# Performance work log

Hardware: AMD Instinct MI355X
Metric: run time of the kernel (lower is better)

## Reference

```python
import jax, jax.numpy as jnp
import numpy as np

N, M, D, G = 8192, 8192, 512, 10

def _embed_distance_matrix(dist):
    # classical MDS embedding: ||e_i - e_j||^2 == dist[i,j]**2
    g = dist.shape[0]
    d2 = dist ** 2
    J = np.eye(g) - np.ones((g, g)) / g
    B = -0.5 * J @ d2 @ J
    w, v = np.linalg.eigh(B)
    w = np.clip(w, 0.0, None)
    return (v * np.sqrt(w)).astype(np.float32)  # [g, g]

def setup_inputs() -> dict:
    key = jax.random.key(0)
    k1, k2, k3, k4 = jax.random.split(key, 4)
    X = jax.random.normal(k1, (N, D), dtype=jnp.float32)
    Z = jax.random.normal(k2, (M, D), dtype=jnp.float32)
    groupsX = jax.random.randint(k3, (N,), 0, G)
    groupsZ = jax.random.randint(k4, (M,), 0, G)
    group_distances = np.ones((G, G)) - np.eye(G)
    embedding = jnp.asarray(_embed_distance_matrix(group_distances))
    return {
        "X": X, "Z": Z,
        "groupsX": groupsX, "groupsZ": groupsZ,
        "embedding": embedding,
        "sigma": jnp.float32(1.0),
        "lengthscale": jnp.float32(1.0),
        "group_diff_param": jnp.float32(1.0),
    }

def _pairwise_sqdist(a, b):
    # ||a_i - b_j||^2 via GEMM; avoids the O(N*M*d) diff tensor
    aa = jnp.sum(a * a, axis=-1)  # [N]
    bb = jnp.sum(b * b, axis=-1)  # [M]
    return aa[:, None] + bb[None, :] - 2.0 * (a @ b.T)  # [N, M]

def reference(X, Z, groupsX, groupsZ, embedding, sigma, lengthscale, group_diff_param):
    p = X.shape[-1]
    ex = embedding[groupsX]  # [N, g]
    ez = embedding[groupsZ]  # [M, g]
    dist = _pairwise_sqdist(X, Z)           # [N, M]
    gdist = _pairwise_sqdist(ex, ez)        # [N, M]
    val = 1.0 / (jnp.abs(group_diff_param) * gdist + 1.0)
    dist_scaled = dist / lengthscale ** 2
    K = sigma ** 2 * jnp.exp(-0.5 * dist_scaled * val) * val ** (0.5 * p)
    return K  # [N, M], matches torch result.transpose(-1, 0)
```

## Files before the change

kernel.cpp:

```cpp
#include <hip/hip_runtime.h>
#include <hip/hip_bf16.h>
#include <cstdint>
#include <cstddef>

#define NROWS 8192
#define MCOLS 8192
#define DDIM  512
#define GRP   10

using bf16x8 = __attribute__((ext_vector_type(8))) short;
using f32x4  = __attribute__((ext_vector_type(4))) float;

typedef const __attribute__((address_space(1))) void* gas_ptr;
typedef __attribute__((address_space(3))) void* las_ptr;

__global__ void prep_tables(const float* __restrict__ emb,
                            const float* __restrict__ sigma_p,
                            const float* __restrict__ ls_p,
                            const float* __restrict__ gdp_p,
                            float* __restrict__ t_tab,
                            float* __restrict__ c2_tab) {
    int t = threadIdx.x;
    if (t >= GRP * GRP) return;
    int a = t / GRP, b = t % GRP;
    float gd = 0.0f;
    for (int g = 0; g < GRP; ++g) {
        float d = emb[a * GRP + g] - emb[b * GRP + g];
        gd += d * d;
    }
    float val = 1.0f / (fabsf(*gdp_p) * gd + 1.0f);
    float ls = *ls_p;
    float sg = *sigma_p;
    t_tab[t]  = -0.5f * val / (ls * ls);
    c2_tab[t] = sg * sg * powf(val, 0.5f * (float)DDIM);
}

__global__ __launch_bounds__(256) void prep_rows(const float* __restrict__ X,
                                                 const float* __restrict__ Z,
                                                 __hip_bfloat16* __restrict__ Xb,
                                                 __hip_bfloat16* __restrict__ Zb,
                                                 float* __restrict__ xx,
                                                 float* __restrict__ zz) {
    int row = blockIdx.x;
    const float* src;
    __hip_bfloat16* dst;
    float* sums;
    int r;
    if (row < NROWS) {
        r = row; src = X + (size_t)r * DDIM; dst = Xb + (size_t)r * DDIM; sums = xx;
    } else {
        r = row - NROWS; src = Z + (size_t)r * DDIM; dst = Zb + (size_t)r * DDIM; sums = zz;
    }
    int t = threadIdx.x;
    float a = src[t];
    float b = src[t + 256];
    dst[t]       = __float2bfloat16(a);
    dst[t + 256] = __float2bfloat16(b);
    float s = a * a + b * b;
    #pragma unroll
    for (int off = 32; off > 0; off >>= 1) s += __shfl_down(s, off, 64);
    __shared__ float ws[4];
    if ((t & 63) == 0) ws[t >> 6] = s;
    __syncthreads();
    if (t == 0) sums[r] = ws[0] + ws[1] + ws[2] + ws[3];
}

__global__ __launch_bounds__(256) void mggp_gemm(
    const __hip_bfloat16* __restrict__ Xb, const __hip_bfloat16* __restrict__ Zb,
    const float* __restrict__ xx, const float* __restrict__ zz,
    const int* __restrict__ gX, const int* __restrict__ gZ,
    const float* __restrict__ t_tab, const float* __restrict__ c2_tab,
    float* __restrict__ out) {

    __shared__ __align__(16) short Al[1024 * 8];
    __shared__ __align__(16) short Bl[1024 * 8];

    const int tid  = threadIdx.x;
    const int lane = tid & 63;
    const int w    = tid >> 6;
    const int wr   = w >> 1;
    const int wc   = w & 1;
    const int m    = lane & 15;
    const int q    = lane >> 4;

    const int brow = blockIdx.y * 128;
    const int bcol = blockIdx.x * 128;

    f32x4 acc[4][4];
    #pragma unroll
    for (int ti = 0; ti < 4; ++ti)
        #pragma unroll
        for (int tj = 0; tj < 4; ++tj)
            #pragma unroll
            for (int e = 0; e < 4; ++e) acc[ti][tj][e] = 0.0f;

    for (int kt = 0; kt < DDIM / 64; ++kt) {
        __syncthreads();
        #pragma unroll
        for (int p = 0; p < 4; ++p) {
            int sbase = (w * 4 + p) * 64;
            int s = sbase + lane;
            int r = s >> 3;
            int o = (s & 7) ^ (r & 7);
            const __hip_bfloat16* ga = Xb + (size_t)(brow + r) * DDIM + kt * 64 + o * 8;
            __builtin_amdgcn_global_load_lds((gas_ptr)ga, (las_ptr)&Al[sbase * 8], 16, 0, 0);
            const __hip_bfloat16* gb = Zb + (size_t)(bcol + r) * DDIM + kt * 64 + o * 8;
            __builtin_amdgcn_global_load_lds((gas_ptr)gb, (las_ptr)&Bl[sbase * 8], 16, 0, 0);
        }
        __syncthreads();

        #pragma unroll
        for (int kk = 0; kk < 2; ++kk) {
            bf16x8 aF[4], bF[4];
            #pragma unroll
            for (int ti = 0; ti < 4; ++ti) {
                int r = wr * 64 + ti * 16 + m;
                int o = kk * 4 + q;
                aF[ti] = *(const bf16x8*)&Al[(r * 8 + (o ^ (r & 7))) * 8];
            }
            #pragma unroll
            for (int tj = 0; tj < 4; ++tj) {
                int r = wc * 64 + tj * 16 + m;
                int o = kk * 4 + q;
                bF[tj] = *(const bf16x8*)&Bl[(r * 8 + (o ^ (r & 7))) * 8];
            }
            #pragma unroll
            for (int ti = 0; ti < 4; ++ti)
                #pragma unroll
                for (int tj = 0; tj < 4; ++tj)
                    acc[ti][tj] = __builtin_amdgcn_mfma_f32_16x16x32_bf16(
                        aF[ti], bF[tj], acc[ti][tj], 0, 0, 0);
        }
    }

    float zzv[4];
    int   gbv[4];
    #pragma unroll
    for (int tj = 0; tj < 4; ++tj) {
        int j = bcol + wc * 64 + tj * 16 + m;
        zzv[tj] = zz[j];
        gbv[tj] = gZ[j];
    }
    #pragma unroll
    for (int ti = 0; ti < 4; ++ti) {
        #pragma unroll
        for (int rg = 0; rg < 4; ++rg) {
            int i = brow + wr * 64 + ti * 16 + q * 4 + rg;
            float xxi = xx[i];
            int   ga  = gX[i] * GRP;
            float* orow = out + (size_t)i * MCOLS + bcol + wc * 64 + m;
            #pragma unroll
            for (int tj = 0; tj < 4; ++tj) {
                float dot  = acc[ti][tj][rg];
                float dist = xxi + zzv[tj] - 2.0f * dot;
                int   idx  = ga + gbv[tj];
                orow[tj * 16] = c2_tab[idx] * expf(dist * t_tab[idx]);
            }
        }
    }
}

extern "C" void kernel_launch(void* const* d_in, const int* in_sizes, int n_in,
                              void* d_out, int out_size, void* d_ws, size_t ws_size,
                              hipStream_t stream) {
    const float* X     = (const float*)d_in[0];
    const float* Z     = (const float*)d_in[1];
    const int*   gX    = (const int*)d_in[2];
    const int*   gZ    = (const int*)d_in[3];
    const float* emb   = (const float*)d_in[4];
    const float* sigma = (const float*)d_in[5];
    const float* ls    = (const float*)d_in[6];
    const float* gdp   = (const float*)d_in[7];

    char* ws = (char*)d_ws;
    const size_t XB_OFF  = 0;
    const size_t ZB_OFF  = XB_OFF + (size_t)NROWS * DDIM * 2;
    const size_t XX_OFF  = ZB_OFF + (size_t)MCOLS * DDIM * 2;
    const size_t ZZ_OFF  = XX_OFF + (size_t)NROWS * 4;
    const size_t TT_OFF  = ZZ_OFF + (size_t)MCOLS * 4;
    const size_t C2_OFF  = TT_OFF + 512;

    __hip_bfloat16* Xb = (__hip_bfloat16*)(ws + XB_OFF);
    __hip_bfloat16* Zb = (__hip_bfloat16*)(ws + ZB_OFF);
    float* xx    = (float*)(ws + XX_OFF);
    float* zz    = (float*)(ws + ZZ_OFF);
    float* t_tab = (float*)(ws + TT_OFF);
    float* c2tab = (float*)(ws + C2_OFF);

    prep_tables<<<1, 128, 0, stream>>>(emb, sigma, ls, gdp, t_tab, c2tab);
    prep_rows<<<2 * NROWS, 256, 0, stream>>>(X, Z, Xb, Zb, xx, zz);
    dim3 grid(MCOLS / 128, NROWS / 128);
    mggp_gemm<<<grid, 256, 0, stream>>>(Xb, Zb, xx, zz, gX, gZ, t_tab, c2tab,
                                        (float*)d_out);
}
```

Measured before the change: 405.0 us.

## Fuse prep kernels, vectorize row prep, swizzle GEMM tiles, use fast exp

```diff
diff --git a/kernel.cpp b/kernel.cpp
--- a/kernel.cpp
+++ b/kernel.cpp
@@ -14,34 +14,36 @@
 typedef const __attribute__((address_space(1))) void* gas_ptr;
 typedef __attribute__((address_space(3))) void* las_ptr;
 
-__global__ void prep_tables(const float* __restrict__ emb,
-                            const float* __restrict__ sigma_p,
-                            const float* __restrict__ ls_p,
-                            const float* __restrict__ gdp_p,
-                            float* __restrict__ t_tab,
-                            float* __restrict__ c2_tab) {
+__global__ __launch_bounds__(256) void prep_all(const float* __restrict__ X,
+                                                const float* __restrict__ Z,
+                                                __hip_bfloat16* __restrict__ Xb,
+                                                __hip_bfloat16* __restrict__ Zb,
+                                                float* __restrict__ xx,
+                                                float* __restrict__ zz,
+                                                const float* __restrict__ emb,
+                                                const float* __restrict__ sigma_p,
+                                                const float* __restrict__ ls_p,
+                                                const float* __restrict__ gdp_p,
+                                                float* __restrict__ t_tab,
+                                                float* __restrict__ c2_tab) {
+    int row = blockIdx.x;
     int t = threadIdx.x;
-    if (t >= GRP * GRP) return;
-    int a = t / GRP, b = t % GRP;
-    float gd = 0.0f;
-    for (int g = 0; g < GRP; ++g) {
-        float d = emb[a * GRP + g] - emb[b * GRP + g];
-        gd += d * d;
-    }
-    float val = 1.0f / (fabsf(*gdp_p) * gd + 1.0f);
-    float ls = *ls_p;
-    float sg = *sigma_p;
-    t_tab[t]  = -0.5f * val / (ls * ls);
-    c2_tab[t] = sg * sg * powf(val, 0.5f * (float)DDIM);
-}
-
-__global__ __launch_bounds__(256) void prep_rows(const float* __restrict__ X,
-                                                 const float* __restrict__ Z,
-                                                 __hip_bfloat16* __restrict__ Xb,
-                                                 __hip_bfloat16* __restrict__ Zb,
-                                                 float* __restrict__ xx,
-                                                 float* __restrict__ zz) {
-    int row = blockIdx.x;
+    if (row == 2 * NROWS) {
+        if (t >= GRP * GRP) return;
+        int a = t / GRP, b = t % GRP;
+        float gd = 0.0f;
+        #pragma unroll
+        for (int g = 0; g < GRP; ++g) {
+            float d = emb[a * GRP + g] - emb[b * GRP + g];
+            gd += d * d;
+        }
+        float val = 1.0f / (fabsf(*gdp_p) * gd + 1.0f);
+        float ls = *ls_p;
+        float sg = *sigma_p;
+        t_tab[t]  = -0.5f * val / (ls * ls);
+        c2_tab[t] = sg * sg * powf(val, 0.5f * (float)DDIM);
+        return;
+    }
     const float* src;
     __hip_bfloat16* dst;
     float* sums;
@@ -51,12 +53,12 @@
     } else {
         r = row - NROWS; src = Z + (size_t)r * DDIM; dst = Zb + (size_t)r * DDIM; sums = zz;
     }
-    int t = threadIdx.x;
-    float a = src[t];
-    float b = src[t + 256];
-    dst[t]       = __float2bfloat16(a);
-    dst[t + 256] = __float2bfloat16(b);
-    float s = a * a + b * b;
+    float2 p = ((const float2*)src)[t];
+    __hip_bfloat162 h;
+    h.x = __float2bfloat16(p.x);
+    h.y = __float2bfloat16(p.y);
+    ((__hip_bfloat162*)dst)[t] = h;
+    float s = p.x * p.x + p.y * p.y;
     #pragma unroll
     for (int off = 32; off > 0; off >>= 1) s += __shfl_down(s, off, 64);
     __shared__ float ws[4];
@@ -83,8 +85,13 @@
     const int m    = lane & 15;
     const int q    = lane >> 4;
 
-    const int brow = blockIdx.y * 128;
-    const int bcol = blockIdx.x * 128;
+    const int lin = blockIdx.x;
+    const int st  = lin >> 6;
+    const int wi  = lin & 63;
+    const int bx  = (st & 7) * 8 + (wi & 7);
+    const int by  = (st >> 3) * 8 + (wi >> 3);
+    const int brow = by * 128;
+    const int bcol = bx * 128;
 
     f32x4 acc[4][4];
     #pragma unroll
@@ -154,7 +161,7 @@
                 float dot  = acc[ti][tj][rg];
                 float dist = xxi + zzv[tj] - 2.0f * dot;
                 int   idx  = ga + gbv[tj];
-                orow[tj * 16] = c2_tab[idx] * expf(dist * t_tab[idx]);
+                orow[tj * 16] = c2_tab[idx] * __expf(dist * t_tab[idx]);
             }
         }
     }
@@ -187,9 +194,8 @@
     float* t_tab = (float*)(ws + TT_OFF);
     float* c2tab = (float*)(ws + C2_OFF);
 
-    prep_tables<<<1, 128, 0, stream>>>(emb, sigma, ls, gdp, t_tab, c2tab);
-    prep_rows<<<2 * NROWS, 256, 0, stream>>>(X, Z, Xb, Zb, xx, zz);
-    dim3 grid(MCOLS / 128, NROWS / 128);
-    mggp_gemm<<<grid, 256, 0, stream>>>(Xb, Zb, xx, zz, gX, gZ, t_tab, c2tab,
+    prep_all<<<2 * NROWS + 1, 256, 0, stream>>>(X, Z, Xb, Zb, xx, zz,
+                                                emb, sigma, ls, gdp, t_tab, c2tab);
+    mggp_gemm<<<4096, 256, 0, stream>>>(Xb, Zb, xx, zz, gX, gZ, t_tab, c2tab,
                                         (float*)d_out);
 }
```

After: 403.3 us. No clear change (-0.4%).
